# Kernel tuning notes

Hardware: AMD Instinct MI355X
Metric: run time of the kernel (lower is better)

Reference implementation:

```python
import jax, jax.numpy as jnp
import numpy as np
from jax import lax

B, L, D_IN, H, RES, BD, D_OUT = 1024, 128, 5, 64, 256, 8, 1


def setup_inputs() -> dict:
    key = jax.random.key(0)
    ks = jax.random.split(key, 14)
    f = jnp.float32
    d = {}
    d["V_noise"] = jax.random.normal(ks[0], (B, D_IN), f)
    d["increments"] = jax.random.normal(ks[1], (B, L, BD), f)
    d["W1"] = jax.random.normal(ks[2], (H, D_IN), f) / np.float32(np.sqrt(D_IN))
    d["b1"] = jnp.zeros((H,), f)
    d["W2"] = jax.random.normal(ks[3], (RES, H), f) / np.float32(np.sqrt(H))
    d["b2"] = jnp.zeros((RES,), f)
    d["rho1"] = jax.random.normal(ks[4], (1, 1), f)
    d["rho2"] = jax.random.normal(ks[5], (1, 1), f)
    d["rho3"] = jax.random.normal(ks[6], (1, 1), f)
    d["rho4"] = jax.random.normal(ks[7], (1, 1), f)
    d["rho5"] = jax.random.normal(ks[8], (1, 1), f)
    # scale reservoir matrices by 1/sqrt(res) so pre-activations are O(1)
    d["B1"] = jax.random.normal(ks[9], (RES, RES), f) / np.float32(np.sqrt(RES))
    d["B2"] = jax.random.normal(ks[10], (BD, RES, RES), f) / np.float32(np.sqrt(RES))
    d["lambda1"] = jax.random.normal(ks[11], (RES, 1), f)
    d["lambda2"] = jax.random.normal(ks[12], (BD, RES, 1), f)
    d["Wr"] = jax.random.normal(ks[13], (D_OUT, RES), f) / np.float32(np.sqrt(RES))
    d["br"] = jnp.zeros((D_OUT,), f)
    return d


def reference(V_noise, increments, W1, b1, W2, b2,
              rho1, rho2, rho3, rho4, rho5,
              B1, B2, lambda1, lambda2, Wr, br):
    act = jnp.tanh
    # initial-condition MLP: [B, D_in] -> [B, RES]
    V = act(V_noise @ W1.T + b1) @ W2.T + b2
    # Brownian path with W[:,0] = 0
    Wp = jnp.cumsum(increments, axis=1).at[:, 0, :].set(0.0)
    dW = Wp[:, 1:] - Wp[:, :-1]          # [B, L-1, BD]
    l1 = lambda1[:, 0]                    # [RES]
    l2 = lambda2[:, :, 0]                 # [BD, RES]
    rho5s = rho5[0, 0]

    def step(r, dw):                      # r: [B, RES], dw: [B, BD]
        drift = act(rho1 * (r @ B1.T) + rho2 * l1)                      # [B, RES]
        diff = act(rho3 * jnp.einsum('kij,bj->bki', B2, r) + rho4 * l2)  # [B, BD, RES]
        rn = r + drift + rho5s * jnp.einsum('bki,bk->bi', diff, dw)
        return rn, rn

    _, Rs = lax.scan(step, V, jnp.swapaxes(dW, 0, 1))  # [L-1, B, RES]
    Rall = jnp.concatenate([V[None], Rs], axis=0)       # [L, B, RES]
    # time-homogeneous linear readout per lag, concatenated along time
    x = Rall @ Wr.T + br                                 # [L, B, D_out]
    out = jnp.transpose(x, (1, 0, 2)).reshape(V.shape[0], Rall.shape[0] * x.shape[-1], 1)
    return out
```

## Files before the change

kernel.cpp:

```cpp
#include <hip/hip_runtime.h>
#include <hip/hip_bf16.h>

#define B_TOT 1024
#define L_T   128
#define DIN   5
#define HD    64
#define RESN  256
#define BDN   8
#define NMAT  9
#define NROWS (NMAT * RESN)
#define PLANE ((size_t)NROWS * RESN)
#define NGRP  16
#define BG    64
#define FPB   16
#define NTHR  256
#define RB_GRP (2 * BG * RESN)
#define WS_RB_OFF  (2 * PLANE * 2)
#define WS_FLAG_OFF (WS_RB_OFF + (size_t)NGRP * RB_GRP * 4)

typedef __attribute__((ext_vector_type(8))) short bf16x8;
typedef __attribute__((ext_vector_type(4))) float f32x4;

__device__ __forceinline__ float fast_tanh(float x) {
    float e = __expf(2.0f * x);
    return 1.0f - 2.0f * __builtin_amdgcn_rcpf(e + 1.0f);
}

__device__ __forceinline__ unsigned pack_hilo(float v) {
    __hip_bfloat16 hi = __float2bfloat16(v);
    __hip_bfloat16 lo = __float2bfloat16(v - __bfloat162float(hi));
    return (unsigned)__builtin_bit_cast(unsigned short, hi) |
           ((unsigned)__builtin_bit_cast(unsigned short, lo) << 16);
}

__device__ __forceinline__ uint4 mall_load4(const unsigned* p) {
    uint4 r;
    asm volatile("global_load_dwordx4 %0, %1, off sc0 sc1" : "=v"(r) : "v"(p));
    return r;
}
__device__ __forceinline__ void mall_store1(unsigned* p, unsigned v) {
    asm volatile("global_store_dword %0, %1, off sc0 sc1" :: "v"(p), "v"(v) : "memory");
}
__device__ __forceinline__ void wait_vm0() {
    asm volatile("s_waitcnt vmcnt(0)" ::: "memory");
}

__global__ void conv_w(const float* __restrict__ B1, const float* __restrict__ B2,
                       __hip_bfloat16* __restrict__ wh, __hip_bfloat16* __restrict__ wl) {
    int idx = blockIdx.x * 256 + threadIdx.x;
    float v = (idx < RESN * RESN) ? B1[idx] : B2[idx - RESN * RESN];
    __hip_bfloat16 h = __float2bfloat16(v);
    wh[idx] = h;
    wl[idx] = __float2bfloat16(v - __bfloat162float(h));
}

__global__ __launch_bounds__(NTHR, 1) void sde_ws(
    const float* __restrict__ Vn,  const float* __restrict__ inc,
    const float* __restrict__ W1,  const float* __restrict__ b1,
    const float* __restrict__ W2,  const float* __restrict__ b2,
    const float* __restrict__ rho1p, const float* __restrict__ rho2p,
    const float* __restrict__ rho3p, const float* __restrict__ rho4p,
    const float* __restrict__ rho5p,
    const float* __restrict__ lam1, const float* __restrict__ lam2,
    const float* __restrict__ Wr,  const float* __restrict__ brp,
    const __hip_bfloat16* __restrict__ wbf,
    unsigned int* __restrict__ rbu,
    unsigned int* __restrict__ flags,
    float* __restrict__ out)
{
    __shared__ __align__(16) short wlds[2][NMAT][8][64][8];
    __shared__ __align__(16) short wrlds[2][8][4][8];
    __shared__ __align__(16) short zfrag[8];

    const int tid  = threadIdx.x;
    const int mt   = tid >> 6;
    const int lane = tid & 63;
    const int n16  = lane & 15;
    const int quad = lane >> 4;
    const int bx   = blockIdx.x;
    const int g    = ((bx & 7) << 1) | (bx >> 7);
    const int fb   = (bx >> 3) & 15;
    const int f0   = fb * FPB;
    const int b0g  = g * BG;
    unsigned int* rbg   = rbu + (size_t)g * RB_GRP;
    unsigned int* flagp = flags + g * 16;

    const float rho1 = rho1p[0], rho2 = rho2p[0], rho3 = rho3p[0],
                rho4 = rho4p[0], rho5 = rho5p[0];
    const float brv = brp[0];

    float* hf  = (float*)&wlds[0][0][0][0][0];
    float* vsh = hf + 64 * 66;
    for (int p = tid; p < BG * HD; p += NTHR) {
        int b = p >> 6, hh = p & 63;
        float s = b1[hh];
        #pragma unroll
        for (int d = 0; d < DIN; ++d) s += Vn[(b0g + b) * DIN + d] * W1[hh * DIN + d];
        hf[b * 66 + hh] = fast_tanh(s);
    }
    __syncthreads();
    for (int p = tid; p < BG * FPB; p += NTHR) {
        int b = p >> 4, f = p & 15;
        float s = b2[f0 + f];
        #pragma unroll 8
        for (int hh = 0; hh < HD; ++hh) s += hf[b * 66 + hh] * W2[(f0 + f) * HD + hh];
        vsh[b * 16 + f] = s;
        mall_store1(&rbg[(0 * BG + b) * RESN + f0 + f], pack_hilo(s));
    }
    __syncthreads();

    float rmast[4];
    #pragma unroll
    for (int rg = 0; rg < 4; ++rg) rmast[rg] = vsh[(16 * mt + 4 * quad + rg) * 16 + n16];
    const float l1c = lam1[f0 + n16];
    float l2c[BDN];
    #pragma unroll
    for (int k = 0; k < BDN; ++k) l2c[k] = lam2[k * RESN + f0 + n16];
    __syncthreads();
    wait_vm0();
    if (tid == 0)
        __hip_atomic_fetch_add(flagp, 1u, __ATOMIC_RELAXED, __HIP_MEMORY_SCOPE_AGENT);

    for (int e = tid; e < 2 * NMAT * 8 * 64; e += NTHR) {
        int l  = e & 63;
        int kk = (e >> 6) & 7;
        int m  = e >> 9;
        int pl = (m >= NMAT) ? 1 : 0;
        int nt = m - pl * NMAT;
        const uint4* src = (const uint4*)(wbf + (size_t)pl * PLANE +
            (size_t)(nt * RESN + f0 + (l & 15)) * RESN + kk * 32 + (l >> 4) * 8);
        *(uint4*)&wlds[pl][nt][kk][l][0] = *src;
    }
    for (int p = tid; p < 512; p += NTHR) {
        int s = p >> 3, j = p & 7;
        int pl = s >> 5, kk = (s >> 2) & 7, q = s & 3;
        float v = Wr[kk * 32 + q * 8 + j];
        __hip_bfloat16 hi = __float2bfloat16(v);
        wrlds[pl][kk][q][j] = pl ? __builtin_bit_cast(short, __float2bfloat16(v - __bfloat162float(hi)))
                                 : __builtin_bit_cast(short, hi);
    }
    if (tid < 8) zfrag[tid] = 0;
    __syncthreads();

    for (int t = 0; t < L_T - 1; ++t) {
        float dwv[4][8];
        #pragma unroll
        for (int rg = 0; rg < 4; ++rg) {
            const size_t bglob = (size_t)(b0g + 16 * mt + 4 * quad + rg) * (L_T * BDN);
            const float4 d0 = *(const float4*)(inc + bglob + (size_t)(t + 1) * BDN);
            const float4 d1 = *(const float4*)(inc + bglob + (size_t)(t + 1) * BDN + 4);
            dwv[rg][0] = d0.x; dwv[rg][1] = d0.y; dwv[rg][2] = d0.z; dwv[rg][3] = d0.w;
            dwv[rg][4] = d1.x; dwv[rg][5] = d1.y; dwv[rg][6] = d1.z; dwv[rg][7] = d1.w;
            if (t == 0) {
                const float4 e0 = *(const float4*)(inc + bglob);
                const float4 e1 = *(const float4*)(inc + bglob + 4);
                dwv[rg][0] += e0.x; dwv[rg][1] += e0.y; dwv[rg][2] += e0.z; dwv[rg][3] += e0.w;
                dwv[rg][4] += e1.x; dwv[rg][5] += e1.y; dwv[rg][6] += e1.z; dwv[rg][7] += e1.w;
            }
        }
        {
            unsigned want = 16u * (unsigned)(t + 1);
            unsigned it = 0;
            while (__hip_atomic_load(flagp, __ATOMIC_RELAXED, __HIP_MEMORY_SCOPE_AGENT) < want) {
                __builtin_amdgcn_s_sleep(1);
                if (++it > (1u << 22)) break;
            }
        }
        const int cur = t & 1, nxt = cur ^ 1;

        uint4 ua[16];
        {
            const unsigned* rbc = rbg + (size_t)(cur * BG + 16 * mt + n16) * RESN + quad * 8;
            #pragma unroll
            for (int kk = 0; kk < 8; ++kk) {
                ua[2 * kk]     = mall_load4(rbc + kk * 32);
                ua[2 * kk + 1] = mall_load4(rbc + kk * 32 + 4);
            }
        }
        wait_vm0();
        bf16x8 afh[8], afl[8];
        #pragma unroll
        for (int kk = 0; kk < 8; ++kk) {
            const uint4 a = ua[2 * kk], b = ua[2 * kk + 1];
            unsigned hw[4], lw[4];
            hw[0] = __builtin_amdgcn_perm(a.y, a.x, 0x05040100u);
            hw[1] = __builtin_amdgcn_perm(a.w, a.z, 0x05040100u);
            hw[2] = __builtin_amdgcn_perm(b.y, b.x, 0x05040100u);
            hw[3] = __builtin_amdgcn_perm(b.w, b.z, 0x05040100u);
            lw[0] = __builtin_amdgcn_perm(a.y, a.x, 0x07060302u);
            lw[1] = __builtin_amdgcn_perm(a.w, a.z, 0x07060302u);
            lw[2] = __builtin_amdgcn_perm(b.y, b.x, 0x07060302u);
            lw[3] = __builtin_amdgcn_perm(b.w, b.z, 0x07060302u);
            afh[kk] = __builtin_bit_cast(bf16x8, *(__attribute__((ext_vector_type(4))) unsigned*)hw);
            afl[kk] = __builtin_bit_cast(bf16x8, *(__attribute__((ext_vector_type(4))) unsigned*)lw);
        }

        f32x4 acc[NMAT] = {};
        #pragma unroll
        for (int kk = 0; kk < 8; ++kk) {
            bf16x8 bh[NMAT], bl[NMAT];
            #pragma unroll
            for (int nt = 0; nt < NMAT; ++nt) {
                bh[nt] = *(const bf16x8*)&wlds[0][nt][kk][lane][0];
                bl[nt] = *(const bf16x8*)&wlds[1][nt][kk][lane][0];
            }
            #pragma unroll
            for (int nt = 0; nt < NMAT; ++nt)
                acc[nt] = __builtin_amdgcn_mfma_f32_16x16x32_bf16(afh[kk], bh[nt], acc[nt], 0, 0, 0);
            #pragma unroll
            for (int nt = 0; nt < NMAT; ++nt)
                acc[nt] = __builtin_amdgcn_mfma_f32_16x16x32_bf16(afl[kk], bh[nt], acc[nt], 0, 0, 0);
            #pragma unroll
            for (int nt = 0; nt < NMAT; ++nt)
                acc[nt] = __builtin_amdgcn_mfma_f32_16x16x32_bf16(afh[kk], bl[nt], acc[nt], 0, 0, 0);
        }

        #pragma unroll
        for (int rg = 0; rg < 4; ++rg) {
            const int bl_ = 16 * mt + 4 * quad + rg;
            float drift = fast_tanh(rho1 * acc[0][rg] + rho2 * l1c);
            float s = 0.0f;
            #pragma unroll
            for (int k = 0; k < BDN; ++k)
                s += fast_tanh(rho3 * acc[1 + k][rg] + rho4 * l2c[k]) * dwv[rg][k];
            float rn = rmast[rg] + drift + rho5 * s;
            rmast[rg] = rn;
            mall_store1(&rbg[(nxt * BG + bl_) * RESN + f0 + n16], pack_hilo(rn));
        }
        wait_vm0();
        __syncthreads();
        if (tid == 0)
            __hip_atomic_fetch_add(flagp, 1u, __ATOMIC_RELAXED, __HIP_MEMORY_SCOPE_AGENT);

        if (fb == 0) {
            f32x4 accw = {};
            const short* ph = (n16 == 0) ? &wrlds[0][0][quad][0] : &zfrag[0];
            const short* pl = (n16 == 0) ? &wrlds[1][0][quad][0] : &zfrag[0];
            const int stp = (n16 == 0) ? 4 * 8 : 0;
            #pragma unroll
            for (int kk = 0; kk < 8; ++kk) {
                bf16x8 wh8 = *(const bf16x8*)(ph + kk * stp);
                bf16x8 wl8 = *(const bf16x8*)(pl + kk * stp);
                accw = __builtin_amdgcn_mfma_f32_16x16x32_bf16(afh[kk], wh8, accw, 0, 0, 0);
                accw = __builtin_amdgcn_mfma_f32_16x16x32_bf16(afl[kk], wh8, accw, 0, 0, 0);
                accw = __builtin_amdgcn_mfma_f32_16x16x32_bf16(afh[kk], wl8, accw, 0, 0, 0);
            }
            if (n16 == 0) {
                #pragma unroll
                for (int rg = 0; rg < 4; ++rg)
                    out[(size_t)(b0g + 16 * mt + 4 * quad + rg) * L_T + t] = accw[rg] + brv;
            }
        }
    }

    if (fb == 0) {
        {
            unsigned want = 16u * (unsigned)L_T;
            unsigned it = 0;
            while (__hip_atomic_load(flagp, __ATOMIC_RELAXED, __HIP_MEMORY_SCOPE_AGENT) < want) {
                __builtin_amdgcn_s_sleep(1);
                if (++it > (1u << 22)) break;
            }
        }
        uint4 ua[16];
        const unsigned* rbc = rbg + (size_t)(1 * BG + 16 * mt + n16) * RESN + quad * 8;
        #pragma unroll
        for (int kk = 0; kk < 8; ++kk) {
            ua[2 * kk]     = mall_load4(rbc + kk * 32);
            ua[2 * kk + 1] = mall_load4(rbc + kk * 32 + 4);
        }
        wait_vm0();
        f32x4 accw = {};
        const short* ph = (n16 == 0) ? &wrlds[0][0][quad][0] : &zfrag[0];
        const short* pl = (n16 == 0) ? &wrlds[1][0][quad][0] : &zfrag[0];
        const int stp = (n16 == 0) ? 4 * 8 : 0;
        #pragma unroll
        for (int kk = 0; kk < 8; ++kk) {
            const uint4 a = ua[2 * kk], b = ua[2 * kk + 1];
            unsigned hw[4], lw[4];
            hw[0] = __builtin_amdgcn_perm(a.y, a.x, 0x05040100u);
            hw[1] = __builtin_amdgcn_perm(a.w, a.z, 0x05040100u);
            hw[2] = __builtin_amdgcn_perm(b.y, b.x, 0x05040100u);
            hw[3] = __builtin_amdgcn_perm(b.w, b.z, 0x05040100u);
            lw[0] = __builtin_amdgcn_perm(a.y, a.x, 0x07060302u);
            lw[1] = __builtin_amdgcn_perm(a.w, a.z, 0x07060302u);
            lw[2] = __builtin_amdgcn_perm(b.y, b.x, 0x07060302u);
            lw[3] = __builtin_amdgcn_perm(b.w, b.z, 0x07060302u);
            bf16x8 ah = __builtin_bit_cast(bf16x8, *(__attribute__((ext_vector_type(4))) unsigned*)hw);
            bf16x8 al = __builtin_bit_cast(bf16x8, *(__attribute__((ext_vector_type(4))) unsigned*)lw);
            bf16x8 wh8 = *(const bf16x8*)(ph + kk * stp);
            bf16x8 wl8 = *(const bf16x8*)(pl + kk * stp);
            accw = __builtin_amdgcn_mfma_f32_16x16x32_bf16(ah, wh8, accw, 0, 0, 0);
            accw = __builtin_amdgcn_mfma_f32_16x16x32_bf16(al, wh8, accw, 0, 0, 0);
            accw = __builtin_amdgcn_mfma_f32_16x16x32_bf16(ah, wl8, accw, 0, 0, 0);
        }
        if (n16 == 0) {
            #pragma unroll
            for (int rg = 0; rg < 4; ++rg)
                out[(size_t)(b0g + 16 * mt + 4 * quad + rg) * L_T + (L_T - 1)] = accw[rg] + brv;
        }
    }
}

extern "C" void kernel_launch(void* const* d_in, const int* in_sizes, int n_in,
                              void* d_out, int out_size, void* d_ws, size_t ws_size,
                              hipStream_t stream) {
    const float* Vn   = (const float*)d_in[0];
    const float* inc  = (const float*)d_in[1];
    const float* W1   = (const float*)d_in[2];
    const float* b1   = (const float*)d_in[3];
    const float* W2   = (const float*)d_in[4];
    const float* b2   = (const float*)d_in[5];
    const float* r1   = (const float*)d_in[6];
    const float* r2   = (const float*)d_in[7];
    const float* r3   = (const float*)d_in[8];
    const float* r4   = (const float*)d_in[9];
    const float* r5   = (const float*)d_in[10];
    const float* B1   = (const float*)d_in[11];
    const float* B2   = (const float*)d_in[12];
    const float* lam1 = (const float*)d_in[13];
    const float* lam2 = (const float*)d_in[14];
    const float* Wr   = (const float*)d_in[15];
    const float* br   = (const float*)d_in[16];

    __hip_bfloat16* wh    = (__hip_bfloat16*)d_ws;
    unsigned int*   rbu   = (unsigned int*)((char*)d_ws + WS_RB_OFF);
    unsigned int*   flags = (unsigned int*)((char*)d_ws + WS_FLAG_OFF);
    float* out = (float*)d_out;

    hipMemsetAsync(flags, 0, NGRP * 16 * sizeof(unsigned int), stream);
    conv_w<<<dim3(NROWS * RESN / 256), dim3(256), 0, stream>>>(B1, B2, wh, wh + PLANE);
    sde_ws<<<dim3(256), dim3(NTHR), 0, stream>>>(
        Vn, inc, W1, b1, W2, b2, r1, r2, r3, r4, r5, lam1, lam2, Wr, br,
        wh, rbu, flags, out);
}
```

Baseline: 907.8 us.

## Replace per-group step barrier with per-wave flags and incremental K-chunk consumption

Each group previously had one shared counter that every block bumped after a block-wide barrier, and consumers waited for all 16 blocks before loading the state. Now each wave owns its own flag, and consumers poll all 64 flags with a ballot. They then load and run the MFMA work for whichever 32-column K-chunks are already ready, and the block-wide __syncthreads per step is removed. The readout MFMA for step t is folded into this incremental loop. This cuts barrier latency and overlaps waiting with compute, but adds more polling loads and control divergence and depends on the ordering of the relaxed per-wave flag protocol.

New measurement: 1.471 ms. 62.0% more time.

```diff
diff --git a/kernel.cpp b/kernel.cpp
--- a/kernel.cpp
+++ b/kernel.cpp
@@ -36,6 +36,11 @@
 __device__ __forceinline__ uint4 mall_load4(const unsigned* p) {
     uint4 r;
     asm volatile("global_load_dwordx4 %0, %1, off sc0 sc1" : "=v"(r) : "v"(p));
+    return r;
+}
+__device__ __forceinline__ unsigned mall_load1(const unsigned* p) {
+    unsigned r;
+    asm volatile("global_load_dword %0, %1, off sc0 sc1" : "=v"(r) : "v"(p));
     return r;
 }
 __device__ __forceinline__ void mall_store1(unsigned* p, unsigned v) {
@@ -83,7 +88,8 @@
     const int f0   = fb * FPB;
     const int b0g  = g * BG;
     unsigned int* rbg   = rbu + (size_t)g * RB_GRP;
-    unsigned int* flagp = flags + g * 16;
+    unsigned int* flagp = flags + g * 64;
+    unsigned int* myflag = flagp + fb * 4 + mt;
 
     const float rho1 = rho1p[0], rho2 = rho2p[0], rho3 = rho3p[0],
                 rho4 = rho4p[0], rho5 = rho5p[0];
@@ -99,14 +105,21 @@
         hf[b * 66 + hh] = fast_tanh(s);
     }
     __syncthreads();
-    for (int p = tid; p < BG * FPB; p += NTHR) {
-        int b = p >> 4, f = p & 15;
-        float s = b2[f0 + f];
-        #pragma unroll 8
-        for (int hh = 0; hh < HD; ++hh) s += hf[b * 66 + hh] * W2[(f0 + f) * HD + hh];
-        vsh[b * 16 + f] = s;
-        mall_store1(&rbg[(0 * BG + b) * RESN + f0 + f], pack_hilo(s));
-    }
+    {
+        int b = 16 * mt + (lane >> 2);
+        #pragma unroll
+        for (int i = 0; i < 4; ++i) {
+            int f = (lane & 3) * 4 + i;
+            float s = b2[f0 + f];
+            #pragma unroll 8
+            for (int hh = 0; hh < HD; ++hh) s += hf[b * 66 + hh] * W2[(f0 + f) * HD + hh];
+            vsh[b * 16 + f] = s;
+            mall_store1(&rbg[(0 * BG + b) * RESN + f0 + f], pack_hilo(s));
+        }
+    }
+    wait_vm0();
+    if (lane == 0)
+        __hip_atomic_fetch_add(myflag, 1u, __ATOMIC_RELAXED, __HIP_MEMORY_SCOPE_AGENT);
     __syncthreads();
 
     float rmast[4];
@@ -117,9 +130,6 @@
     #pragma unroll
     for (int k = 0; k < BDN; ++k) l2c[k] = lam2[k * RESN + f0 + n16];
     __syncthreads();
-    wait_vm0();
-    if (tid == 0)
-        __hip_atomic_fetch_add(flagp, 1u, __ATOMIC_RELAXED, __HIP_MEMORY_SCOPE_AGENT);
 
     for (int e = tid; e < 2 * NMAT * 8 * 64; e += NTHR) {
         int l  = e & 63;
@@ -141,6 +151,11 @@
     }
     if (tid < 8) zfrag[tid] = 0;
     __syncthreads();
+
+    const short* ph = (n16 == 0) ? &wrlds[0][0][quad][0] : &zfrag[0];
+    const short* pw = (n16 == 0) ? &wrlds[1][0][quad][0] : &zfrag[0];
+    const int    stp = (n16 == 0) ? 4 * 8 : 0;
+    const unsigned* fladdr = (const unsigned*)(flagp + ((lane & 15) * 4 + mt));
 
     for (int t = 0; t < L_T - 1; ++t) {
         float dwv[4][8];
@@ -158,61 +173,75 @@
                 dwv[rg][4] += e1.x; dwv[rg][5] += e1.y; dwv[rg][6] += e1.z; dwv[rg][7] += e1.w;
             }
         }
-        {
-            unsigned want = 16u * (unsigned)(t + 1);
-            unsigned it = 0;
-            while (__hip_atomic_load(flagp, __ATOMIC_RELAXED, __HIP_MEMORY_SCOPE_AGENT) < want) {
+        const unsigned want = (unsigned)(t + 1);
+        const int cur = t & 1, nxt = cur ^ 1;
+        const unsigned* rbc = rbg + (size_t)(cur * BG + 16 * mt + n16) * RESN + quad * 8;
+
+        f32x4 acc[NMAT] = {};
+        f32x4 accw = {};
+        unsigned done = 0, guard = 0;
+        while (done != 0xffu) {
+            unsigned fv = mall_load1(fladdr);
+            wait_vm0();
+            unsigned long long bm = __ballot(fv >= want);
+            unsigned m16 = (unsigned)bm & (unsigned)(bm >> 16) &
+                           (unsigned)(bm >> 32) & (unsigned)(bm >> 48) & 0xffffu;
+            unsigned pr = m16 & (m16 >> 1);
+            unsigned kkm = 0;
+            #pragma unroll
+            for (int kk = 0; kk < 8; ++kk) kkm |= ((pr >> (2 * kk)) & 1u) << kk;
+            kkm &= ~done;
+            if (kkm == 0) {
                 __builtin_amdgcn_s_sleep(1);
-                if (++it > (1u << 22)) break;
+                if (++guard > (1u << 20)) break;
+                continue;
             }
-        }
-        const int cur = t & 1, nxt = cur ^ 1;
-
-        uint4 ua[16];
-        {
-            const unsigned* rbc = rbg + (size_t)(cur * BG + 16 * mt + n16) * RESN + quad * 8;
-            #pragma unroll
-            for (int kk = 0; kk < 8; ++kk) {
-                ua[2 * kk]     = mall_load4(rbc + kk * 32);
-                ua[2 * kk + 1] = mall_load4(rbc + kk * 32 + 4);
-            }
-        }
-        wait_vm0();
-        bf16x8 afh[8], afl[8];
-        #pragma unroll
-        for (int kk = 0; kk < 8; ++kk) {
-            const uint4 a = ua[2 * kk], b = ua[2 * kk + 1];
-            unsigned hw[4], lw[4];
-            hw[0] = __builtin_amdgcn_perm(a.y, a.x, 0x05040100u);
-            hw[1] = __builtin_amdgcn_perm(a.w, a.z, 0x05040100u);
-            hw[2] = __builtin_amdgcn_perm(b.y, b.x, 0x05040100u);
-            hw[3] = __builtin_amdgcn_perm(b.w, b.z, 0x05040100u);
-            lw[0] = __builtin_amdgcn_perm(a.y, a.x, 0x07060302u);
-            lw[1] = __builtin_amdgcn_perm(a.w, a.z, 0x07060302u);
-            lw[2] = __builtin_amdgcn_perm(b.y, b.x, 0x07060302u);
-            lw[3] = __builtin_amdgcn_perm(b.w, b.z, 0x07060302u);
-            afh[kk] = __builtin_bit_cast(bf16x8, *(__attribute__((ext_vector_type(4))) unsigned*)hw);
-            afl[kk] = __builtin_bit_cast(bf16x8, *(__attribute__((ext_vector_type(4))) unsigned*)lw);
-        }
-
-        f32x4 acc[NMAT] = {};
-        #pragma unroll
-        for (int kk = 0; kk < 8; ++kk) {
-            bf16x8 bh[NMAT], bl[NMAT];
-            #pragma unroll
-            for (int nt = 0; nt < NMAT; ++nt) {
-                bh[nt] = *(const bf16x8*)&wlds[0][nt][kk][lane][0];
-                bl[nt] = *(const bf16x8*)&wlds[1][nt][kk][lane][0];
-            }
-            #pragma unroll
-            for (int nt = 0; nt < NMAT; ++nt)
-                acc[nt] = __builtin_amdgcn_mfma_f32_16x16x32_bf16(afh[kk], bh[nt], acc[nt], 0, 0, 0);
-            #pragma unroll
-            for (int nt = 0; nt < NMAT; ++nt)
-                acc[nt] = __builtin_amdgcn_mfma_f32_16x16x32_bf16(afl[kk], bh[nt], acc[nt], 0, 0, 0);
-            #pragma unroll
-            for (int nt = 0; nt < NMAT; ++nt)
-                acc[nt] = __builtin_amdgcn_mfma_f32_16x16x32_bf16(afh[kk], bl[nt], acc[nt], 0, 0, 0);
+            uint4 ua[16];
+            #pragma unroll
+            for (int kk = 0; kk < 8; ++kk)
+                if (kkm & (1u << kk)) {
+                    ua[2 * kk]     = mall_load4(rbc + kk * 32);
+                    ua[2 * kk + 1] = mall_load4(rbc + kk * 32 + 4);
+                }
+            wait_vm0();
+            #pragma unroll
+            for (int kk = 0; kk < 8; ++kk)
+                if (kkm & (1u << kk)) {
+                    const uint4 a = ua[2 * kk], b = ua[2 * kk + 1];
+                    unsigned hw[4], lw[4];
+                    hw[0] = __builtin_amdgcn_perm(a.y, a.x, 0x05040100u);
+                    hw[1] = __builtin_amdgcn_perm(a.w, a.z, 0x05040100u);
+                    hw[2] = __builtin_amdgcn_perm(b.y, b.x, 0x05040100u);
+                    hw[3] = __builtin_amdgcn_perm(b.w, b.z, 0x05040100u);
+                    lw[0] = __builtin_amdgcn_perm(a.y, a.x, 0x07060302u);
+                    lw[1] = __builtin_amdgcn_perm(a.w, a.z, 0x07060302u);
+                    lw[2] = __builtin_amdgcn_perm(b.y, b.x, 0x07060302u);
+                    lw[3] = __builtin_amdgcn_perm(b.w, b.z, 0x07060302u);
+                    bf16x8 afh = __builtin_bit_cast(bf16x8, *(__attribute__((ext_vector_type(4))) unsigned*)hw);
+                    bf16x8 afl = __builtin_bit_cast(bf16x8, *(__attribute__((ext_vector_type(4))) unsigned*)lw);
+                    #pragma unroll
+                    for (int nt = 0; nt < NMAT; ++nt) {
+                        bf16x8 bh = *(const bf16x8*)&wlds[0][nt][kk][lane][0];
+                        bf16x8 bl = *(const bf16x8*)&wlds[1][nt][kk][lane][0];
+                        acc[nt] = __builtin_amdgcn_mfma_f32_16x16x32_bf16(afh, bh, acc[nt], 0, 0, 0);
+                        acc[nt] = __builtin_amdgcn_mfma_f32_16x16x32_bf16(afl, bh, acc[nt], 0, 0, 0);
+                        acc[nt] = __builtin_amdgcn_mfma_f32_16x16x32_bf16(afh, bl, acc[nt], 0, 0, 0);
+                    }
+                    if (fb == 0) {
+                        bf16x8 wh8 = *(const bf16x8*)(ph + kk * stp);
+                        bf16x8 wl8 = *(const bf16x8*)(pw + kk * stp);
+                        accw = __builtin_amdgcn_mfma_f32_16x16x32_bf16(afh, wh8, accw, 0, 0, 0);
+                        accw = __builtin_amdgcn_mfma_f32_16x16x32_bf16(afl, wh8, accw, 0, 0, 0);
+                        accw = __builtin_amdgcn_mfma_f32_16x16x32_bf16(afh, wl8, accw, 0, 0, 0);
+                    }
+                }
+            done |= kkm;
+        }
+
+        if (fb == 0 && n16 == 0) {
+            #pragma unroll
+            for (int rg = 0; rg < 4; ++rg)
+                out[(size_t)(b0g + 16 * mt + 4 * quad + rg) * L_T + t] = accw[rg] + brv;
         }
 
         #pragma unroll
@@ -228,71 +257,61 @@
             mall_store1(&rbg[(nxt * BG + bl_) * RESN + f0 + n16], pack_hilo(rn));
         }
         wait_vm0();
-        __syncthreads();
-        if (tid == 0)
-            __hip_atomic_fetch_add(flagp, 1u, __ATOMIC_RELAXED, __HIP_MEMORY_SCOPE_AGENT);
-
-        if (fb == 0) {
-            f32x4 accw = {};
-            const short* ph = (n16 == 0) ? &wrlds[0][0][quad][0] : &zfrag[0];
-            const short* pl = (n16 == 0) ? &wrlds[1][0][quad][0] : &zfrag[0];
-            const int stp = (n16 == 0) ? 4 * 8 : 0;
-            #pragma unroll
-            for (int kk = 0; kk < 8; ++kk) {
-                bf16x8 wh8 = *(const bf16x8*)(ph + kk * stp);
-                bf16x8 wl8 = *(const bf16x8*)(pl + kk * stp);
-                accw = __builtin_amdgcn_mfma_f32_16x16x32_bf16(afh[kk], wh8, accw, 0, 0, 0);
-                accw = __builtin_amdgcn_mfma_f32_16x16x32_bf16(afl[kk], wh8, accw, 0, 0, 0);
-                accw = __builtin_amdgcn_mfma_f32_16x16x32_bf16(afh[kk], wl8, accw, 0, 0, 0);
+        if (lane == 0)
+            __hip_atomic_fetch_add(myflag, 1u, __ATOMIC_RELAXED, __HIP_MEMORY_SCOPE_AGENT);
+    }
+
+    if (fb == 0) {
+        const unsigned want = (unsigned)L_T;
+        const unsigned* rbc = rbg + (size_t)(1 * BG + 16 * mt + n16) * RESN + quad * 8;
+        f32x4 accw = {};
+        unsigned done = 0, guard = 0;
+        while (done != 0xffu) {
+            unsigned fv = mall_load1(fladdr);
+            wait_vm0();
+            unsigned long long bm = __ballot(fv >= want);
+            unsigned m16 = (unsigned)bm & (unsigned)(bm >> 16) &
+                           (unsigned)(bm >> 32) & (unsigned)(bm >> 48) & 0xffffu;
+            unsigned pr = m16 & (m16 >> 1);
+            unsigned kkm = 0;
+            #pragma unroll
+            for (int kk = 0; kk < 8; ++kk) kkm |= ((pr >> (2 * kk)) & 1u) << kk;
+            kkm &= ~done;
+            if (kkm == 0) {
+                __builtin_amdgcn_s_sleep(1);
+                if (++guard > (1u << 20)) break;
+                continue;
             }
-            if (n16 == 0) {
-                #pragma unroll
-                for (int rg = 0; rg < 4; ++rg)
-                    out[(size_t)(b0g + 16 * mt + 4 * quad + rg) * L_T + t] = accw[rg] + brv;
-            }
-        }
-    }
-
-    if (fb == 0) {
-        {
-            unsigned want = 16u * (unsigned)L_T;
-            unsigned it = 0;
-            while (__hip_atomic_load(flagp, __ATOMIC_RELAXED, __HIP_MEMORY_SCOPE_AGENT) < want) {
-                __builtin_amdgcn_s_sleep(1);
-                if (++it > (1u << 22)) break;
-            }
-        }
-        uint4 ua[16];
-        const unsigned* rbc = rbg + (size_t)(1 * BG + 16 * mt + n16) * RESN + quad * 8;
-        #pragma unroll
-        for (int kk = 0; kk < 8; ++kk) {
-            ua[2 * kk]     = mall_load4(rbc + kk * 32);
-            ua[2 * kk + 1] = mall_load4(rbc + kk * 32 + 4);
-        }
-        wait_vm0();
-        f32x4 accw = {};
-        const short* ph = (n16 == 0) ? &wrlds[0][0][quad][0] : &zfrag[0];
-        const short* pl = (n16 == 0) ? &wrlds[1][0][quad][0] : &zfrag[0];
-        const int stp = (n16 == 0) ? 4 * 8 : 0;
-        #pragma unroll
-        for (int kk = 0; kk < 8; ++kk) {
-            const uint4 a = ua[2 * kk], b = ua[2 * kk + 1];
-            unsigned hw[4], lw[4];
-            hw[0] = __builtin_amdgcn_perm(a.y, a.x, 0x05040100u);
-            hw[1] = __builtin_amdgcn_perm(a.w, a.z, 0x05040100u);
-            hw[2] = __builtin_amdgcn_perm(b.y, b.x, 0x05040100u);
-            hw[3] = __builtin_amdgcn_perm(b.w, b.z, 0x05040100u);
-            lw[0] = __builtin_amdgcn_perm(a.y, a.x, 0x07060302u);
-            lw[1] = __builtin_amdgcn_perm(a.w, a.z, 0x07060302u);
-            lw[2] = __builtin_amdgcn_perm(b.y, b.x, 0x07060302u);
-            lw[3] = __builtin_amdgcn_perm(b.w, b.z, 0x07060302u);
-            bf16x8 ah = __builtin_bit_cast(bf16x8, *(__attribute__((ext_vector_type(4))) unsigned*)hw);
-            bf16x8 al = __builtin_bit_cast(bf16x8, *(__attribute__((ext_vector_type(4))) unsigned*)lw);
-            bf16x8 wh8 = *(const bf16x8*)(ph + kk * stp);
-            bf16x8 wl8 = *(const bf16x8*)(pl + kk * stp);
-            accw = __builtin_amdgcn_mfma_f32_16x16x32_bf16(ah, wh8, accw, 0, 0, 0);
-            accw = __builtin_amdgcn_mfma_f32_16x16x32_bf16(al, wh8, accw, 0, 0, 0);
-            accw = __builtin_amdgcn_mfma_f32_16x16x32_bf16(ah, wl8, accw, 0, 0, 0);
+            uint4 ua[16];
+            #pragma unroll
+            for (int kk = 0; kk < 8; ++kk)
+                if (kkm & (1u << kk)) {
+                    ua[2 * kk]     = mall_load4(rbc + kk * 32);
+                    ua[2 * kk + 1] = mall_load4(rbc + kk * 32 + 4);
+                }
+            wait_vm0();
+            #pragma unroll
+            for (int kk = 0; kk < 8; ++kk)
+                if (kkm & (1u << kk)) {
+                    const uint4 a = ua[2 * kk], b = ua[2 * kk + 1];
+                    unsigned hw[4], lw[4];
+                    hw[0] = __builtin_amdgcn_perm(a.y, a.x, 0x05040100u);
+                    hw[1] = __builtin_amdgcn_perm(a.w, a.z, 0x05040100u);
+                    hw[2] = __builtin_amdgcn_perm(b.y, b.x, 0x05040100u);
+                    hw[3] = __builtin_amdgcn_perm(b.w, b.z, 0x05040100u);
+                    lw[0] = __builtin_amdgcn_perm(a.y, a.x, 0x07060302u);
+                    lw[1] = __builtin_amdgcn_perm(a.w, a.z, 0x07060302u);
+                    lw[2] = __builtin_amdgcn_perm(b.y, b.x, 0x07060302u);
+                    lw[3] = __builtin_amdgcn_perm(b.w, b.z, 0x07060302u);
+                    bf16x8 afh = __builtin_bit_cast(bf16x8, *(__attribute__((ext_vector_type(4))) unsigned*)hw);
+                    bf16x8 afl = __builtin_bit_cast(bf16x8, *(__attribute__((ext_vector_type(4))) unsigned*)lw);
+                    bf16x8 wh8 = *(const bf16x8*)(ph + kk * stp);
+                    bf16x8 wl8 = *(const bf16x8*)(pw + kk * stp);
+                    accw = __builtin_amdgcn_mfma_f32_16x16x32_bf16(afh, wh8, accw, 0, 0, 0);
+                    accw = __builtin_amdgcn_mfma_f32_16x16x32_bf16(afl, wh8, accw, 0, 0, 0);
+                    accw = __builtin_amdgcn_mfma_f32_16x16x32_bf16(afh, wl8, accw, 0, 0, 0);
+                }
+            done |= kkm;
         }
         if (n16 == 0) {
             #pragma unroll
@@ -328,7 +347,7 @@
     unsigned int*   flags = (unsigned int*)((char*)d_ws + WS_FLAG_OFF);
     float* out = (float*)d_out;
 
-    hipMemsetAsync(flags, 0, NGRP * 16 * sizeof(unsigned int), stream);
+    hipMemsetAsync(flags, 0, NGRP * 64 * sizeof(unsigned int), stream);
     conv_w<<<dim3(NROWS * RESN / 256), dim3(256), 0, stream>>>(B1, B2, wh, wh + PLANE);
     sde_ws<<<dim3(256), dim3(NTHR), 0, stream>>>(
         Vn, inc, W1, b1, W2, b2, r1, r2, r3, r4, r5, lam1, lam2, Wr, br,
```

## Replace per-group counter barrier with per-wave flags and rotate readout block

Applied to the files above, without the earlier changes.

Replaces the single shared atomic counter per batch group, which every block incremented after a __syncthreads, with one flag per wave (per feature block and M-tile) on its own cache line. Each wave polls all 16 peer flags for its tile with one load per lane and a ballot, so waves only wait for the producers of the rows they actually read. The block-wide barrier inside the time loop is removed. The readout MFMA work rotates across feature blocks by time step instead of always falling on block 0. This removes contention on one atomic and cuts sync latency on the serial time-step chain, but adds more polling traffic and a larger flag array.

After: 873.1 us. 1.04x faster.

```diff
diff --git a/kernel.cpp b/kernel.cpp
--- a/kernel.cpp
+++ b/kernel.cpp
@@ -17,6 +17,7 @@
 #define RB_GRP (2 * BG * RESN)
 #define WS_RB_OFF  (2 * PLANE * 2)
 #define WS_FLAG_OFF (WS_RB_OFF + (size_t)NGRP * RB_GRP * 4)
+#define FLAGS_PER_GRP 1024
 
 typedef __attribute__((ext_vector_type(8))) short bf16x8;
 typedef __attribute__((ext_vector_type(4))) float f32x4;
@@ -38,11 +39,27 @@
     asm volatile("global_load_dwordx4 %0, %1, off sc0 sc1" : "=v"(r) : "v"(p));
     return r;
 }
+__device__ __forceinline__ unsigned mall_load1(const unsigned* p) {
+    unsigned r;
+    asm volatile("global_load_dword %0, %1, off sc0 sc1" : "=v"(r) : "v"(p));
+    return r;
+}
 __device__ __forceinline__ void mall_store1(unsigned* p, unsigned v) {
     asm volatile("global_store_dword %0, %1, off sc0 sc1" :: "v"(p), "v"(v) : "memory");
 }
 __device__ __forceinline__ void wait_vm0() {
     asm volatile("s_waitcnt vmcnt(0)" ::: "memory");
+}
+
+__device__ __forceinline__ void spin_all(const unsigned* fladdr, unsigned want) {
+    unsigned guard = 0;
+    for (;;) {
+        unsigned fv = mall_load1(fladdr);
+        wait_vm0();
+        if (__ballot(fv < want) == 0ull) break;
+        __builtin_amdgcn_s_sleep(1);
+        if (++guard > (1u << 20)) break;
+    }
 }
 
 __global__ void conv_w(const float* __restrict__ B1, const float* __restrict__ B2,
@@ -82,8 +99,10 @@
     const int fb   = (bx >> 3) & 15;
     const int f0   = fb * FPB;
     const int b0g  = g * BG;
-    unsigned int* rbg   = rbu + (size_t)g * RB_GRP;
-    unsigned int* flagp = flags + g * 16;
+    unsigned int* rbg    = rbu + (size_t)g * RB_GRP;
+    unsigned int* flagp  = flags + g * FLAGS_PER_GRP;
+    unsigned int* myflag = flagp + (fb * 4 + mt) * 16;
+    const unsigned* fladdr = (const unsigned*)(flagp + ((lane & 15) * 4 + mt) * 16);
 
     const float rho1 = rho1p[0], rho2 = rho2p[0], rho3 = rho3p[0],
                 rho4 = rho4p[0], rho5 = rho5p[0];
@@ -99,15 +118,21 @@
         hf[b * 66 + hh] = fast_tanh(s);
     }
     __syncthreads();
-    for (int p = tid; p < BG * FPB; p += NTHR) {
-        int b = p >> 4, f = p & 15;
-        float s = b2[f0 + f];
-        #pragma unroll 8
-        for (int hh = 0; hh < HD; ++hh) s += hf[b * 66 + hh] * W2[(f0 + f) * HD + hh];
-        vsh[b * 16 + f] = s;
-        mall_store1(&rbg[(0 * BG + b) * RESN + f0 + f], pack_hilo(s));
-    }
-    __syncthreads();
+    {
+        int b = 16 * mt + (lane >> 2);
+        #pragma unroll
+        for (int i = 0; i < 4; ++i) {
+            int f = (lane & 3) * 4 + i;
+            float s = b2[f0 + f];
+            #pragma unroll 8
+            for (int hh = 0; hh < HD; ++hh) s += hf[b * 66 + hh] * W2[(f0 + f) * HD + hh];
+            vsh[b * 16 + f] = s;
+            mall_store1(&rbg[(0 * BG + b) * RESN + f0 + f], pack_hilo(s));
+        }
+    }
+    wait_vm0();
+    if (lane == 0)
+        __hip_atomic_fetch_add(myflag, 1u, __ATOMIC_RELAXED, __HIP_MEMORY_SCOPE_AGENT);
 
     float rmast[4];
     #pragma unroll
@@ -117,9 +142,6 @@
     #pragma unroll
     for (int k = 0; k < BDN; ++k) l2c[k] = lam2[k * RESN + f0 + n16];
     __syncthreads();
-    wait_vm0();
-    if (tid == 0)
-        __hip_atomic_fetch_add(flagp, 1u, __ATOMIC_RELAXED, __HIP_MEMORY_SCOPE_AGENT);
 
     for (int e = tid; e < 2 * NMAT * 8 * 64; e += NTHR) {
         int l  = e & 63;
@@ -141,6 +163,10 @@
     }
     if (tid < 8) zfrag[tid] = 0;
     __syncthreads();
+
+    const short* ph = (n16 == 0) ? &wrlds[0][0][quad][0] : &zfrag[0];
+    const short* pw = (n16 == 0) ? &wrlds[1][0][quad][0] : &zfrag[0];
+    const int    stp = (n16 == 0) ? 4 * 8 : 0;
 
     for (int t = 0; t < L_T - 1; ++t) {
         float dwv[4][8];
@@ -158,15 +184,9 @@
                 dwv[rg][4] += e1.x; dwv[rg][5] += e1.y; dwv[rg][6] += e1.z; dwv[rg][7] += e1.w;
             }
         }
-        {
-            unsigned want = 16u * (unsigned)(t + 1);
-            unsigned it = 0;
-            while (__hip_atomic_load(flagp, __ATOMIC_RELAXED, __HIP_MEMORY_SCOPE_AGENT) < want) {
-                __builtin_amdgcn_s_sleep(1);
-                if (++it > (1u << 22)) break;
-            }
-        }
+        spin_all(fladdr, (unsigned)(t + 1));
         const int cur = t & 1, nxt = cur ^ 1;
+        const int lead = t & 15;
 
         uint4 ua[16];
         {
@@ -228,19 +248,15 @@
             mall_store1(&rbg[(nxt * BG + bl_) * RESN + f0 + n16], pack_hilo(rn));
         }
         wait_vm0();
-        __syncthreads();
-        if (tid == 0)
-            __hip_atomic_fetch_add(flagp, 1u, __ATOMIC_RELAXED, __HIP_MEMORY_SCOPE_AGENT);
-
-        if (fb == 0) {
+        if (lane == 0)
+            __hip_atomic_fetch_add(myflag, 1u, __ATOMIC_RELAXED, __HIP_MEMORY_SCOPE_AGENT);
+
+        if (fb == lead) {
             f32x4 accw = {};
-            const short* ph = (n16 == 0) ? &wrlds[0][0][quad][0] : &zfrag[0];
-            const short* pl = (n16 == 0) ? &wrlds[1][0][quad][0] : &zfrag[0];
-            const int stp = (n16 == 0) ? 4 * 8 : 0;
             #pragma unroll
             for (int kk = 0; kk < 8; ++kk) {
                 bf16x8 wh8 = *(const bf16x8*)(ph + kk * stp);
-                bf16x8 wl8 = *(const bf16x8*)(pl + kk * stp);
+                bf16x8 wl8 = *(const bf16x8*)(pw + kk * stp);
                 accw = __builtin_amdgcn_mfma_f32_16x16x32_bf16(afh[kk], wh8, accw, 0, 0, 0);
                 accw = __builtin_amdgcn_mfma_f32_16x16x32_bf16(afl[kk], wh8, accw, 0, 0, 0);
                 accw = __builtin_amdgcn_mfma_f32_16x16x32_bf16(afh[kk], wl8, accw, 0, 0, 0);
@@ -253,15 +269,8 @@
         }
     }
 
-    if (fb == 0) {
-        {
-            unsigned want = 16u * (unsigned)L_T;
-            unsigned it = 0;
-            while (__hip_atomic_load(flagp, __ATOMIC_RELAXED, __HIP_MEMORY_SCOPE_AGENT) < want) {
-                __builtin_amdgcn_s_sleep(1);
-                if (++it > (1u << 22)) break;
-            }
-        }
+    if (fb == 15) {
+        spin_all(fladdr, (unsigned)L_T);
         uint4 ua[16];
         const unsigned* rbc = rbg + (size_t)(1 * BG + 16 * mt + n16) * RESN + quad * 8;
         #pragma unroll
@@ -271,9 +280,6 @@
         }
         wait_vm0();
         f32x4 accw = {};
-        const short* ph = (n16 == 0) ? &wrlds[0][0][quad][0] : &zfrag[0];
-        const short* pl = (n16 == 0) ? &wrlds[1][0][quad][0] : &zfrag[0];
-        const int stp = (n16 == 0) ? 4 * 8 : 0;
         #pragma unroll
         for (int kk = 0; kk < 8; ++kk) {
             const uint4 a = ua[2 * kk], b = ua[2 * kk + 1];
@@ -289,7 +295,7 @@
             bf16x8 ah = __builtin_bit_cast(bf16x8, *(__attribute__((ext_vector_type(4))) unsigned*)hw);
             bf16x8 al = __builtin_bit_cast(bf16x8, *(__attribute__((ext_vector_type(4))) unsigned*)lw);
             bf16x8 wh8 = *(const bf16x8*)(ph + kk * stp);
-            bf16x8 wl8 = *(const bf16x8*)(pl + kk * stp);
+            bf16x8 wl8 = *(const bf16x8*)(pw + kk * stp);
             accw = __builtin_amdgcn_mfma_f32_16x16x32_bf16(ah, wh8, accw, 0, 0, 0);
             accw = __builtin_amdgcn_mfma_f32_16x16x32_bf16(al, wh8, accw, 0, 0, 0);
             accw = __builtin_amdgcn_mfma_f32_16x16x32_bf16(ah, wl8, accw, 0, 0, 0);
@@ -328,7 +334,7 @@
     unsigned int*   flags = (unsigned int*)((char*)d_ws + WS_FLAG_OFF);
     float* out = (float*)d_out;
 
-    hipMemsetAsync(flags, 0, NGRP * 16 * sizeof(unsigned int), stream);
+    hipMemsetAsync(flags, 0, NGRP * FLAGS_PER_GRP * sizeof(unsigned int), stream);
     conv_w<<<dim3(NROWS * RESN / 256), dim3(256), 0, stream>>>(B1, B2, wh, wh + PLANE);
     sde_ws<<<dim3(256), dim3(NTHR), 0, stream>>>(
         Vn, inc, W1, b1, W2, b2, r1, r2, r3, r4, r5, lam1, lam2, Wr, br,
```
